# Kernel tuning notes

Hardware: AMD Instinct MI355X
Metric: run time of the kernel (lower is better)

The kernel has to match this reference:

```python
import jax, jax.numpy as jnp
import numpy as np

LN_EPS = 1e-12
K_TOP = 32  # k_top_device, n_devices=1


def _layer_norm(x, g, b):
    mu = jnp.mean(x, axis=-1, keepdims=True)
    var = jnp.mean(jnp.square(x - mu), axis=-1, keepdims=True)
    return (x - mu) * jax.lax.rsqrt(var + LN_EPS) * g + b


def setup_inputs() -> dict:
    key = jax.random.key(0)
    ks = jax.random.split(key, 10)
    B, T, H = 4, 512, 768        # batch, n_tokens, hidden
    NM = 128                      # n_mentions
    ROWS, VPR, KD = 16384, 64, 128  # memory table: 1M slots, key_dim 128
    return dict(
        encoded_input=jax.random.normal(ks[0], (B, T, H), jnp.float32),
        mention_batch_positions=jax.random.randint(ks[1], (NM,), 0, B),
        mention_start_positions=jax.random.randint(ks[2], (NM,), 0, T),
        mention_end_positions=jax.random.randint(ks[3], (NM,), 0, T),
        mention_mask=jnp.ones((NM,), jnp.float32),
        memory_keys=jax.random.normal(ks[4], (ROWS, VPR, KD), jnp.float32) * 0.05,
        memory_entity_ids=jax.random.randint(ks[5], (ROWS * VPR,), 0, 1000000),
        query_w=jax.random.normal(ks[6], (2 * H, KD), jnp.float32) * 0.02,
        query_b=jnp.zeros((KD,), jnp.float32),
        update_w=jax.random.normal(ks[7], (KD, H), jnp.float32) * 0.02,
        update_b=jnp.zeros((H,), jnp.float32),
        ln_gamma=jnp.ones((H,), jnp.float32),
        ln_beta=jnp.zeros((H,), jnp.float32),
    )


def reference(encoded_input, mention_batch_positions, mention_start_positions,
              mention_end_positions, mention_mask, memory_keys,
              memory_entity_ids, query_w, query_b, update_w, update_b,
              ln_gamma, ln_beta):
    rows, vpr, kd = memory_keys.shape
    # gather mention start/end token encodings (matmul_2d_index_select equiv)
    start_enc = encoded_input[mention_batch_positions, mention_start_positions]
    end_enc = encoded_input[mention_batch_positions, mention_end_positions]
    # query projection: Dense(2H -> key_dim)
    queries = jnp.concatenate((start_enc, end_enc), axis=-1) @ query_w + query_b
    q_sg = jax.lax.stop_gradient(queries)  # search uses stop_gradient queries
    # top-k similarity: scores over all memory slots [q, rows, vpr]
    scores = jnp.einsum('qd,rvd->qrv', q_sg, memory_keys)
    within_idx = jnp.argmax(scores, axis=-1)            # [q, rows]
    row_scores = jnp.max(scores, axis=-1)               # [q, rows]
    _, top_rows = jax.lax.top_k(row_scores, K_TOP)      # [q, k]
    top_within = jnp.take_along_axis(within_idx, top_rows, axis=-1)
    top_ids = top_rows * vpr + top_within               # flat memory ids [q, k]
    top_keys = memory_keys.reshape(rows * vpr, kd)[top_ids]  # [q, k, d]
    top_values = top_keys  # memory_values is None -> keys are values
    # attention with gradients through queries and gathered keys
    top_scores_wg = jnp.einsum('qd,qkd->qk', queries, top_keys)
    attn = jax.nn.softmax(top_scores_wg, axis=-1)
    retrieved = jnp.einsum('qk,qkd->qd', attn, top_values)
    retrieved = retrieved * mention_mask[:, None]
    # additive retrieval update + layer norm
    update = retrieved @ update_w + update_b            # [q, H]
    updated = encoded_input.at[
        mention_batch_positions, mention_start_positions].add(update)
    return _layer_norm(updated, ln_gamma, ln_beta)
```

## Files before the change

kernel.cpp:

```cpp
#include <hip/hip_runtime.h>
#include <hip/hip_bf16.h>

#define NM 128
#define HD 768
#define TT 512
#define KD 128
#define NROWS 16384
#define VPR 64
#define KTOP 32
#define K2_BLOCKS 2048
#define NEG_INF -3.402823466e38f

typedef __bf16 bf16x8 __attribute__((ext_vector_type(8)));
typedef float  f32x4  __attribute__((ext_vector_type(4)));

__device__ __forceinline__ unsigned short f2bf(float f) {
    __bf16 h = (__bf16)f;
    return __builtin_bit_cast(unsigned short, h);
}

__global__ __launch_bounds__(256) void k1_queries(
    const float* __restrict__ enc, const int* __restrict__ mb,
    const int* __restrict__ msp, const int* __restrict__ mep,
    const float* __restrict__ qw, const float* __restrict__ qb,
    float* __restrict__ q_f32, unsigned short* __restrict__ q_bf16)
{
    int q = blockIdx.x;
    int b = mb[q], s = msp[q], e = mep[q];
    __shared__ float encs[2 * HD];
    const float* srow = enc + ((size_t)b * TT + s) * HD;
    const float* erow = enc + ((size_t)b * TT + e) * HD;
    for (int i = threadIdx.x; i < HD; i += 256) {
        encs[i]      = srow[i];
        encs[HD + i] = erow[i];
    }
    __syncthreads();
    int d = threadIdx.x & 127;
    int h = threadIdx.x >> 7;
    const float* w  = qw + (size_t)(h * HD) * KD + d;
    const float* ev = encs + h * HD;
    float acc = 0.f;
#pragma unroll 8
    for (int i = 0; i < HD; ++i) acc = fmaf(ev[i], w[(size_t)i * KD], acc);
    __shared__ float part[256];
    part[threadIdx.x] = acc;
    __syncthreads();
    if (threadIdx.x < 128) {
        float v = part[threadIdx.x] + part[threadIdx.x + 128] + qb[d];
        q_f32[q * KD + d] = v;
        unsigned byteoff = ((unsigned)(q * 256 + d * 2)) ^ (((unsigned)(q & 7)) << 4);
        q_bf16[byteoff >> 1] = f2bf(v);
    }
}

__global__ __launch_bounds__(256) void k2_scores(
    const float* __restrict__ mkeys, const unsigned short* __restrict__ q_bf16,
    float* __restrict__ scores_t, unsigned char* __restrict__ widx_t)
{
    __shared__ __attribute__((aligned(16))) unsigned short qs[NM * KD];
    __shared__ __attribute__((aligned(16))) unsigned short ks[VPR * KD];
    {
        const uint4* src = (const uint4*)q_bf16;
        uint4* dst = (uint4*)qs;
#pragma unroll
        for (int i = 0; i < 8; ++i) dst[i * 256 + threadIdx.x] = src[i * 256 + threadIdx.x];
    }
    int lane = threadIdx.x & 63;
    int wave = threadIdx.x >> 6;

    for (int r = blockIdx.x; r < NROWS; r += K2_BLOCKS) {
        __syncthreads();
        const float4* src = (const float4*)(mkeys + (size_t)r * (VPR * KD));
        float4 v[8];
#pragma unroll
        for (int i = 0; i < 8; ++i) v[i] = src[i * 256 + threadIdx.x];
#pragma unroll
        for (int i = 0; i < 8; ++i) {
            int fidx = (i * 256 + threadIdx.x) * 4;
            int slot = fidx >> 7, dd = fidx & 127;
            ushort4 u;
            u.x = f2bf(v[i].x); u.y = f2bf(v[i].y);
            u.z = f2bf(v[i].z); u.w = f2bf(v[i].w);
            unsigned byteoff = ((unsigned)(slot * 256 + dd * 2)) ^ (((unsigned)(slot & 7)) << 4);
            *(ushort4*)((char*)ks + byteoff) = u;
        }
        __syncthreads();
        f32x4 acc[2][4];
        f32x4 zero = {0.f, 0.f, 0.f, 0.f};
#pragma unroll
        for (int qt = 0; qt < 2; ++qt)
#pragma unroll
            for (int st = 0; st < 4; ++st) acc[qt][st] = zero;
#pragma unroll
        for (int kk = 0; kk < 4; ++kk) {
            int kbase = kk * 32 + (lane >> 4) * 8;
            bf16x8 a[2], bb[4];
#pragma unroll
            for (int qt = 0; qt < 2; ++qt) {
                int qrow = (2 * wave + qt) * 16 + (lane & 15);
                unsigned byteoff = ((unsigned)(qrow * 256 + kbase * 2)) ^ (((unsigned)(qrow & 7)) << 4);
                a[qt] = *(const bf16x8*)((const char*)qs + byteoff);
            }
#pragma unroll
            for (int st = 0; st < 4; ++st) {
                int slot = st * 16 + (lane & 15);
                unsigned byteoff = ((unsigned)(slot * 256 + kbase * 2)) ^ (((unsigned)(slot & 7)) << 4);
                bb[st] = *(const bf16x8*)((const char*)ks + byteoff);
            }
#pragma unroll
            for (int qt = 0; qt < 2; ++qt)
#pragma unroll
                for (int st = 0; st < 4; ++st)
                    acc[qt][st] = __builtin_amdgcn_mfma_f32_16x16x32_bf16(a[qt], bb[st], acc[qt][st], 0, 0, 0);
        }
#pragma unroll
        for (int qt = 0; qt < 2; ++qt) {
#pragma unroll
            for (int reg = 0; reg < 4; ++reg) {
                float m = acc[qt][0][reg];
                int  mi = (lane & 15);
#pragma unroll
                for (int st = 1; st < 4; ++st) {
                    float vv = acc[qt][st][reg];
                    int   vi = st * 16 + (lane & 15);
                    if (vv > m) { m = vv; mi = vi; }
                }
#pragma unroll
                for (int delta = 1; delta < 16; delta <<= 1) {
                    float om = __shfl_xor(m, delta);
                    int   oi = __shfl_xor(mi, delta);
                    if (om > m || (om == m && oi < mi)) { m = om; mi = oi; }
                }
                if ((lane & 15) == 0) {
                    int qrow = (2 * wave + qt) * 16 + (lane >> 4) * 4 + reg;
                    scores_t[(size_t)r * NM + qrow] = m;
                    widx_t[(size_t)r * NM + qrow] = (unsigned char)mi;
                }
            }
        }
    }
}

__global__ __launch_bounds__(256) void k3_topk_attn(
    const float* __restrict__ scores_t, const unsigned char* __restrict__ widx_t,
    const float* __restrict__ mkeys, const float* __restrict__ q_f32,
    const float* __restrict__ mask, const float* __restrict__ uw,
    const float* __restrict__ ub, float* __restrict__ upd)
{
    int q = blockIdx.x;
    int tid = threadIdx.x;
    int lane = tid & 63, wave = tid >> 6;
    __shared__ float sc[NROWS];
    __shared__ float cmax[256];
    __shared__ int   cidx[256];
    __shared__ int   toprows[KTOP];
    __shared__ float keys[KTOP][KD];
    __shared__ float sk[KTOP];
    __shared__ float attn[KTOP];
    __shared__ float retr[KD];
    __shared__ int   bestc;
    __shared__ float wval[4];
    __shared__ int   wchk[4];

#pragma unroll 8
    for (int jj = 0; jj < 64; ++jj) {
        int i = jj * 256 + tid;
        sc[i] = scores_t[(size_t)i * NM + q];
    }
    __syncthreads();
    {
        float m = NEG_INF; int mi = 0;
        for (int jj = 0; jj < 64; ++jj) {
            int j = (jj + tid) & 63;
            int i = tid * 64 + j;
            float vv = sc[i];
            if (vv > m || (vv == m && i < mi)) { m = vv; mi = i; }
        }
        cmax[tid] = m; cidx[tid] = mi;
    }
    __syncthreads();
    for (int it = 0; it < KTOP; ++it) {
        float m = cmax[tid]; int c = tid;
#pragma unroll
        for (int delta = 1; delta < 64; delta <<= 1) {
            float om = __shfl_xor(m, delta);
            int   oc = __shfl_xor(c, delta);
            if (om > m || (om == m && oc < c)) { m = om; c = oc; }
        }
        if (lane == 0) { wval[wave] = m; wchk[wave] = c; }
        __syncthreads();
        if (tid == 0) {
            float bm = wval[0]; int bc = wchk[0];
            for (int w2 = 1; w2 < 4; ++w2)
                if (wval[w2] > bm || (wval[w2] == bm && wchk[w2] < bc)) { bm = wval[w2]; bc = wchk[w2]; }
            int row = cidx[bc];
            toprows[it] = row;
            sc[row] = NEG_INF;
            bestc = bc;
        }
        __syncthreads();
        if (wave == 0) {
            int bc = bestc;
            int i  = bc * 64 + lane;
            float m2 = sc[i]; int mi2 = i;
#pragma unroll
            for (int delta = 1; delta < 64; delta <<= 1) {
                float om = __shfl_xor(m2, delta);
                int   oi = __shfl_xor(mi2, delta);
                if (om > m2 || (om == m2 && oi < mi2)) { m2 = om; mi2 = oi; }
            }
            if (lane == 0) { cmax[bc] = m2; cidx[bc] = mi2; }
        }
        __syncthreads();
    }
    for (int k = wave; k < KTOP; k += 4) {
        int row = toprows[k];
        int wid = widx_t[(size_t)row * NM + q];
        const float* kp = mkeys + ((size_t)row * VPR + wid) * KD;
        keys[k][lane]      = kp[lane];
        keys[k][lane + 64] = kp[lane + 64];
    }
    __syncthreads();
    const float* qv = q_f32 + q * KD;
    for (int k = wave; k < KTOP; k += 4) {
        float p = qv[lane] * keys[k][lane] + qv[lane + 64] * keys[k][lane + 64];
#pragma unroll
        for (int delta = 1; delta < 64; delta <<= 1) p += __shfl_xor(p, delta);
        if (lane == 0) sk[k] = p;
    }
    __syncthreads();
    if (tid < 64) {
        float vv = (tid < KTOP) ? sk[tid] : NEG_INF;
        float mx = vv;
#pragma unroll
        for (int delta = 1; delta < 64; delta <<= 1) mx = fmaxf(mx, __shfl_xor(mx, delta));
        float e = (tid < KTOP) ? __expf(vv - mx) : 0.f;
        float ssum = e;
#pragma unroll
        for (int delta = 1; delta < 64; delta <<= 1) ssum += __shfl_xor(ssum, delta);
        if (tid < KTOP) attn[tid] = e / ssum;
    }
    __syncthreads();
    if (tid < KD) {
        float rsum = 0.f;
#pragma unroll
        for (int k = 0; k < KTOP; ++k) rsum = fmaf(attn[k], keys[k][tid], rsum);
        retr[tid] = rsum * mask[q];
    }
    __syncthreads();
    {
        float u0 = ub[tid], u1 = ub[tid + 256], u2 = ub[tid + 512];
        for (int kd2 = 0; kd2 < KD; ++kd2) {
            float rv = retr[kd2];
            const float* wr = uw + (size_t)kd2 * HD;
            u0 = fmaf(rv, wr[tid],       u0);
            u1 = fmaf(rv, wr[tid + 256], u1);
            u2 = fmaf(rv, wr[tid + 512], u2);
        }
        upd[(size_t)q * HD + tid]       = u0;
        upd[(size_t)q * HD + tid + 256] = u1;
        upd[(size_t)q * HD + tid + 512] = u2;
    }
}

__global__ __launch_bounds__(256) void k4_scatter_ln(
    const float* __restrict__ enc, const int* __restrict__ mb, const int* __restrict__ msp,
    const float* __restrict__ upd, const float* __restrict__ gamma,
    const float* __restrict__ beta, float* __restrict__ out)
{
    int tok = blockIdx.x;
    int b = tok >> 9, t = tok & 511;
    int tid = threadIdx.x;
    int lane = tid & 63, wave = tid >> 6;
    __shared__ int mbs[NM], mss[NM];
    if (tid < NM) { mbs[tid] = mb[tid]; mss[tid] = msp[tid]; }
    __syncthreads();
    const float* x = enc + (size_t)tok * HD;
    float x0 = x[tid], x1 = x[tid + 256], x2 = x[tid + 512];
    for (int q = 0; q < NM; ++q) {
        if (mbs[q] == b && mss[q] == t) {
            const float* u = upd + (size_t)q * HD;
            x0 += u[tid]; x1 += u[tid + 256]; x2 += u[tid + 512];
        }
    }
    __shared__ float redA[4], redB[4];
    float s = x0 + x1 + x2;
#pragma unroll
    for (int delta = 1; delta < 64; delta <<= 1) s += __shfl_xor(s, delta);
    if (lane == 0) redA[wave] = s;
    __syncthreads();
    float mu = (redA[0] + redA[1] + redA[2] + redA[3]) * (1.f / 768.f);
    float d0 = x0 - mu, d1 = x1 - mu, d2 = x2 - mu;
    float s2 = d0 * d0 + d1 * d1 + d2 * d2;
#pragma unroll
    for (int delta = 1; delta < 64; delta <<= 1) s2 += __shfl_xor(s2, delta);
    if (lane == 0) redB[wave] = s2;
    __syncthreads();
    float var = (redB[0] + redB[1] + redB[2] + redB[3]) * (1.f / 768.f);
    float rs = rsqrtf(var + 1e-12f);
    float* o = out + (size_t)tok * HD;
    o[tid]       = d0 * rs * gamma[tid]       + beta[tid];
    o[tid + 256] = d1 * rs * gamma[tid + 256] + beta[tid + 256];
    o[tid + 512] = d2 * rs * gamma[tid + 512] + beta[tid + 512];
}

extern "C" void kernel_launch(void* const* d_in, const int* in_sizes, int n_in,
                              void* d_out, int out_size, void* d_ws, size_t ws_size,
                              hipStream_t stream) {
    const float* enc   = (const float*)d_in[0];
    const int*   mb    = (const int*)d_in[1];
    const int*   msp   = (const int*)d_in[2];
    const int*   mep   = (const int*)d_in[3];
    const float* mask  = (const float*)d_in[4];
    const float* mkeys = (const float*)d_in[5];
    const float* qw    = (const float*)d_in[7];
    const float* qb    = (const float*)d_in[8];
    const float* uw    = (const float*)d_in[9];
    const float* ub    = (const float*)d_in[10];
    const float* gamma = (const float*)d_in[11];
    const float* beta  = (const float*)d_in[12];
    float* out = (float*)d_out;

    char* ws = (char*)d_ws;
    float*          q_f32    = (float*)(ws);
    unsigned short* q_bf16   = (unsigned short*)(ws + 65536);
    float*          upd      = (float*)(ws + 98304);
    float*          scores_t = (float*)(ws + 491520);
    unsigned char*  widx_t   = (unsigned char*)(ws + 8880128);

    k1_queries<<<dim3(NM), dim3(256), 0, stream>>>(enc, mb, msp, mep, qw, qb, q_f32, q_bf16);
    k2_scores<<<dim3(K2_BLOCKS), dim3(256), 0, stream>>>(mkeys, q_bf16, scores_t, widx_t);
    k3_topk_attn<<<dim3(NM), dim3(256), 0, stream>>>(scores_t, widx_t, mkeys, q_f32, mask, uw, ub, upd);
    k4_scatter_ln<<<dim3(4 * TT), dim3(256), 0, stream>>>(enc, mb, msp, upd, gamma, beta, out);
}
```

Before: 879.9 us.

## Prefetch next key row in k2 and transpose scores for coalesced k3 loads

k2_scores now issues the global loads for the next memory-key row into registers before running the MFMA compute on the current row, overlapping load latency with compute. It also sets a minimum occupancy of 3 blocks per CU in the launch bounds. A new transpose kernel turns the row-major [rows, queries] score matrix into a query-major layout. k3 can then read each query's 16K scores with contiguous float4 loads instead of strided scalar reads. The cost is an extra kernel launch plus an additional 8 MB write and read of the scores, and higher register pressure in k2.

```diff
diff --git a/kernel.cpp b/kernel.cpp
--- a/kernel.cpp
+++ b/kernel.cpp
@@ -9,6 +9,7 @@
 #define VPR 64
 #define KTOP 32
 #define K2_BLOCKS 2048
+#define TR_ROWS 64
 #define NEG_INF -3.402823466e38f
 
 typedef __bf16 bf16x8 __attribute__((ext_vector_type(8)));
@@ -53,7 +54,7 @@
     }
 }
 
-__global__ __launch_bounds__(256) void k2_scores(
+__global__ __launch_bounds__(256, 3) void k2_scores(
     const float* __restrict__ mkeys, const unsigned short* __restrict__ q_bf16,
     float* __restrict__ scores_t, unsigned char* __restrict__ widx_t)
 {
@@ -65,18 +66,22 @@
 #pragma unroll
         for (int i = 0; i < 8; ++i) dst[i * 256 + threadIdx.x] = src[i * 256 + threadIdx.x];
     }
-    int lane = threadIdx.x & 63;
-    int wave = threadIdx.x >> 6;
+    int tid = threadIdx.x;
+    int lane = tid & 63;
+    int wave = tid >> 6;
+
+    float4 v[8];
+    {
+        const float4* s0 = (const float4*)(mkeys + (size_t)blockIdx.x * (VPR * KD));
+#pragma unroll
+        for (int i = 0; i < 8; ++i) v[i] = s0[i * 256 + tid];
+    }
 
     for (int r = blockIdx.x; r < NROWS; r += K2_BLOCKS) {
         __syncthreads();
-        const float4* src = (const float4*)(mkeys + (size_t)r * (VPR * KD));
-        float4 v[8];
-#pragma unroll
-        for (int i = 0; i < 8; ++i) v[i] = src[i * 256 + threadIdx.x];
 #pragma unroll
         for (int i = 0; i < 8; ++i) {
-            int fidx = (i * 256 + threadIdx.x) * 4;
+            int fidx = (i * 256 + tid) * 4;
             int slot = fidx >> 7, dd = fidx & 127;
             ushort4 u;
             u.x = f2bf(v[i].x); u.y = f2bf(v[i].y);
@@ -85,6 +90,12 @@
             *(ushort4*)((char*)ks + byteoff) = u;
         }
         __syncthreads();
+        int rn = r + K2_BLOCKS;
+        if (rn < NROWS) {
+            const float4* s1 = (const float4*)(mkeys + (size_t)rn * (VPR * KD));
+#pragma unroll
+            for (int i = 0; i < 8; ++i) v[i] = s1[i * 256 + tid];
+        }
         f32x4 acc[2][4];
         f32x4 zero = {0.f, 0.f, 0.f, 0.f};
 #pragma unroll
@@ -141,8 +152,37 @@
     }
 }
 
+__global__ __launch_bounds__(256) void k2b_transpose(
+    const float* __restrict__ st, float* __restrict__ sq)
+{
+    __shared__ float tile[TR_ROWS][133];
+    int r0 = blockIdx.x * TR_ROWS;
+    int tid = threadIdx.x;
+    const float4* src = (const float4*)(st + (size_t)r0 * NM);
+#pragma unroll
+    for (int i = 0; i < 8; ++i) {
+        float4 f = src[i * 256 + tid];
+        int fi = (i * 256 + tid) * 4;
+        int rr = fi >> 7, q = fi & 127;
+        tile[rr][q]     = f.x;
+        tile[rr][q + 1] = f.y;
+        tile[rr][q + 2] = f.z;
+        tile[rr][q + 3] = f.w;
+    }
+    __syncthreads();
+    int rr0 = (tid & 15) * 4;
+#pragma unroll
+    for (int j = 0; j < 8; ++j) {
+        int q = j * 16 + (tid >> 4);
+        float4 o;
+        o.x = tile[rr0][q]; o.y = tile[rr0 + 1][q];
+        o.z = tile[rr0 + 2][q]; o.w = tile[rr0 + 3][q];
+        *(float4*)(sq + (size_t)q * NROWS + r0 + rr0) = o;
+    }
+}
+
 __global__ __launch_bounds__(256) void k3_topk_attn(
-    const float* __restrict__ scores_t, const unsigned char* __restrict__ widx_t,
+    const float* __restrict__ scores_q, const unsigned char* __restrict__ widx_t,
     const float* __restrict__ mkeys, const float* __restrict__ q_f32,
     const float* __restrict__ mask, const float* __restrict__ uw,
     const float* __restrict__ ub, float* __restrict__ upd)
@@ -162,10 +202,14 @@
     __shared__ float wval[4];
     __shared__ int   wchk[4];
 
-#pragma unroll 8
-    for (int jj = 0; jj < 64; ++jj) {
-        int i = jj * 256 + tid;
-        sc[i] = scores_t[(size_t)i * NM + q];
+    {
+        const float4* srcq = (const float4*)(scores_q + (size_t)q * NROWS);
+#pragma unroll
+        for (int jj = 0; jj < 16; ++jj) {
+            float4 f = srcq[jj * 256 + tid];
+            int i = (jj * 256 + tid) * 4;
+            *(float4*)(sc + i) = f;
+        }
     }
     __syncthreads();
     {
@@ -327,9 +371,11 @@
     float*          upd      = (float*)(ws + 98304);
     float*          scores_t = (float*)(ws + 491520);
     unsigned char*  widx_t   = (unsigned char*)(ws + 8880128);
+    float*          scores_q = (float*)(ws + 10977280);
 
     k1_queries<<<dim3(NM), dim3(256), 0, stream>>>(enc, mb, msp, mep, qw, qb, q_f32, q_bf16);
     k2_scores<<<dim3(K2_BLOCKS), dim3(256), 0, stream>>>(mkeys, q_bf16, scores_t, widx_t);
-    k3_topk_attn<<<dim3(NM), dim3(256), 0, stream>>>(scores_t, widx_t, mkeys, q_f32, mask, uw, ub, upd);
+    k2b_transpose<<<dim3(NROWS / TR_ROWS), dim3(256), 0, stream>>>(scores_t, scores_q);
+    k3_topk_attn<<<dim3(NM), dim3(256), 0, stream>>>(scores_q, widx_t, mkeys, q_f32, mask, uw, ub, upd);
     k4_scatter_ln<<<dim3(4 * TT), dim3(256), 0, stream>>>(enc, mb, msp, upd, gamma, beta, out);
 }
```

Result: no change. 862.8 us (-1.9%).
